# Kernel optimization log

Measured on AMD Instinct MI355X. Metric: run time of the kernel, lower is better.

## Reference

```python
import jax, jax.numpy as jnp
import numpy as np

N = 100000
E = 400000
NFEAT, NHID, NOUT, NHEAD = 128, 64, 128, 4
HIDDEN = NHID * NHEAD  # 256
SLOPE = 0.2


def gat_conv(x, src, dst, W, a_src, a_dst, b, concat):
    """PyG-style GATConv (eval mode, self-loops already appended to src/dst).
    x: [N, Fin]; W: [Fin, H*C]; a_src/a_dst: [H, C]; b: [H*C] or [C]."""
    H, C = a_src.shape
    h = (x @ W).reshape(N, H, C)                      # [N,H,C]
    al_s = (h * a_src).sum(-1)                        # [N,H] per-node src score
    al_d = (h * a_dst).sum(-1)                        # [N,H] per-node dst score
    e = jax.nn.leaky_relu(al_s[src] + al_d[dst], SLOPE)  # [Et,H]
    # segment softmax over incoming edges of each dst node
    m = jax.ops.segment_max(e, dst, num_segments=N)
    m = jnp.where(jnp.isfinite(m), m, 0.0)
    ex = jnp.exp(e - m[dst])
    denom = jax.ops.segment_sum(ex, dst, num_segments=N)
    alpha = ex / (denom[dst] + 1e-16)                 # [Et,H]
    msg = alpha[:, :, None] * h[src]                  # [Et,H,C]
    out = jax.ops.segment_sum(msg, dst, num_segments=N)  # [N,H,C]
    out = out.reshape(N, H * C) if concat else out.mean(axis=1)
    return out + b


def setup_inputs() -> dict:
    key = jax.random.key(0)
    ks = jax.random.split(key, 16)
    x = jax.random.normal(ks[0], (N, NFEAT), dtype=jnp.float32)
    edge_index = jax.random.randint(ks[1], (2, E), 0, N, dtype=jnp.int64)
    s = 0.1
    inp = {
        'x': x, 'edge_index': edge_index,
        # layer 0: nfeat -> nhid x nhead (concat)
        'W0': jax.random.normal(ks[2], (NFEAT, HIDDEN), jnp.float32) * s,
        'as0': jax.random.normal(ks[3], (NHEAD, NHID), jnp.float32) * s,
        'ad0': jax.random.normal(ks[4], (NHEAD, NHID), jnp.float32) * s,
        'b0': jnp.zeros((HIDDEN,), jnp.float32),
        # layer 1: hidden -> nhid x nhead (concat)
        'W1': jax.random.normal(ks[5], (HIDDEN, HIDDEN), jnp.float32) * s,
        'as1': jax.random.normal(ks[6], (NHEAD, NHID), jnp.float32) * s,
        'ad1': jax.random.normal(ks[7], (NHEAD, NHID), jnp.float32) * s,
        'b1': jnp.zeros((HIDDEN,), jnp.float32),
        # output layer: hidden -> nout, heads=1, concat=False
        'W2': jax.random.normal(ks[8], (HIDDEN, NOUT), jnp.float32) * s,
        'as2': jax.random.normal(ks[9], (1, NOUT), jnp.float32) * s,
        'ad2': jax.random.normal(ks[10], (1, NOUT), jnp.float32) * s,
        'b2': jnp.zeros((NOUT,), jnp.float32),
    }
    return inp


def reference(x, edge_index, W0, as0, ad0, b0, W1, as1, ad1, b1, W2, as2, ad2, b2):
    # PyG GATConv adds self-loops by default; edge set is shared across layers.
    loop = jnp.arange(N, dtype=edge_index.dtype)
    src = jnp.concatenate([edge_index[0], loop])
    dst = jnp.concatenate([edge_index[1], loop])
    # dropout inactive in eval mode
    h = jax.nn.elu(gat_conv(x, src, dst, W0, as0, ad0, b0, concat=True))
    h = jax.nn.elu(gat_conv(h, src, dst, W1, as1, ad1, b1, concat=True))
    out = gat_conv(h, src, dst, W2, as2, ad2, b2, concat=False)
    return out
```

## Files before the change

### kernel.cpp

```cpp
#include <hip/hip_runtime.h>
#include <cmath>

#define NN 100000
#define EE 400000
#define SLOPE 0.2f
#define MAXDEG 32

typedef __attribute__((ext_vector_type(8))) short short8;
typedef __attribute__((ext_vector_type(4))) float floatx4;

__device__ __forceinline__ float b2f(ushort u) {
    union { unsigned int i; float f; } v; v.i = ((unsigned int)u) << 16; return v.f;
}
__device__ __forceinline__ ushort f2b(float f) {
    union { float f; unsigned int i; } v; v.f = f;
    unsigned int r = v.i + 0x7FFFu + ((v.i >> 16) & 1u);
    return (ushort)(r >> 16);
}

__device__ __forceinline__ void gload16(const ushort* g, ushort* l) {
    __builtin_amdgcn_global_load_lds((const __attribute__((address_space(1))) void*)g,
                                     (__attribute__((address_space(3))) void*)l, 16, 0, 0);
}

__global__ __launch_bounds__(256) void prep(int* __restrict__ cnt,
                                            float* __restrict__ als2, float* __restrict__ ald2,
                                            const float* __restrict__ W0, const float* __restrict__ W1,
                                            const float* __restrict__ W2,
                                            ushort* __restrict__ Wt0, ushort* __restrict__ Wt1,
                                            ushort* __restrict__ Wt2) {
    int idx = blockIdx.x * 256 + threadIdx.x;
    if (idx < 25000) {
        ((int4*)cnt)[idx] = make_int4(0, 0, 0, 0);
    } else if (idx < 50000) {
        ((float4*)als2)[idx - 25000] = make_float4(0.f, 0.f, 0.f, 0.f);
    } else if (idx < 75000) {
        ((float4*)ald2)[idx - 50000] = make_float4(0.f, 0.f, 0.f, 0.f);
    } else {
        int j = idx - 75000;
        if (j < 32768) {
            int n = j >> 7, k = j & 127;
            Wt0[j] = f2b(W0[(size_t)k * 256 + n]);
        } else if (j < 98304) {
            int t = j - 32768;
            int n = t >> 8, k = t & 255;
            Wt1[t] = f2b(W1[(size_t)k * 256 + n]);
        } else if (j < 131072) {
            int t = j - 98304;
            int n = t >> 8, k = t & 255;
            Wt2[t] = f2b(W2[(size_t)k * 128 + n]);
        }
    }
}

__global__ __launch_bounds__(256) void bucket_scatter(const int* __restrict__ ei,
                                                      int* __restrict__ cnt,
                                                      int* __restrict__ bucket) {
    int e = blockIdx.x * 256 + threadIdx.x;
    if (e < EE) {
        int d = ei[EE + e];
        int p = atomicAdd(&cnt[d], 1);
        if (p < MAXDEG) bucket[(d << 5) + p] = ei[e];
    }
}

template <bool CVT>
__global__ __launch_bounds__(256) void gemm_bf16(const void* __restrict__ Avoid,
                                                 const ushort* __restrict__ Bt,
                                                 ushort* __restrict__ C,
                                                 int M, int K, int N, int paired,
                                                 const float* __restrict__ asf,
                                                 const float* __restrict__ adf,
                                                 float* __restrict__ als,
                                                 float* __restrict__ ald,
                                                 int H, int lgC) {
    __shared__ __attribute__((aligned(16))) ushort As[2 * 128 * 64];
    __shared__ __attribute__((aligned(16))) ushort Bs[2 * 128 * 64];
    int tid = threadIdx.x;
    int GMc = (M + 127) >> 7;
    int bmi, bni;
    if (paired) {
        int g = blockIdx.x >> 4, ii = blockIdx.x & 15;
        bmi = g * 8 + (ii & 7);
        bni = ii >> 3;
        if (bmi >= GMc) return;
    } else {
        bmi = blockIdx.x; bni = 0;
    }
    int bm = bmi * 128, bn = bni * 128;
    int wave = tid >> 6, lane = tid & 63;
    int wm = (wave >> 1) * 64, wn = (wave & 1) * 64;

    floatx4 acc[4][4];
#pragma unroll
    for (int i = 0; i < 4; i++)
#pragma unroll
        for (int j = 0; j < 4; j++) acc[i][j] = (floatx4)0.f;

    int rsub = lane >> 3;
    int klog8 = ((lane & 7) ^ rsub) * 8;
    ushort* ldsA = &As[wave * 512];
    ushort* ldsB = &Bs[wave * 512];
    const ushort* bS = Bt + (size_t)(bn + wave * 8 + rsub) * K + klog8;
    const ushort* aS = nullptr;
    if (!CVT) aS = (const ushort*)Avoid + (size_t)(bm + wave * 8 + rsub) * K + klog8;
    const float* Af = (const float*)Avoid;

    int frow = lane & 15;
    int q = lane >> 4;
    int f7 = frow & 7;

    int nt = K >> 6;
    int cur = 0;

    if constexpr (CVT) {
#pragma unroll
        for (int i = 0; i < 4; i++) {
            int arow = bm + wave * 8 + i * 32 + rsub;
            float4 f0 = make_float4(0.f, 0.f, 0.f, 0.f), f1 = f0;
            if (arow < M) {
                const float4* ap = (const float4*)(Af + (size_t)arow * K + klog8);
                f0 = ap[0]; f1 = ap[1];
            }
            uint4 pk;
            pk.x = (uint)f2b(f0.x) | ((uint)f2b(f0.y) << 16);
            pk.y = (uint)f2b(f0.z) | ((uint)f2b(f0.w) << 16);
            pk.z = (uint)f2b(f1.x) | ((uint)f2b(f1.y) << 16);
            pk.w = (uint)f2b(f1.z) | ((uint)f2b(f1.w) << 16);
            *(uint4*)&ldsA[i * 2048 + lane * 8] = pk;
            gload16(bS + (size_t)i * 32 * K, ldsB + i * 2048);
        }
    } else {
#pragma unroll
        for (int i = 0; i < 4; i++) {
            gload16(aS + (size_t)i * 32 * K, ldsA + i * 2048);
            gload16(bS + (size_t)i * 32 * K, ldsB + i * 2048);
        }
    }
    __syncthreads();

    for (int t = 0; t < nt; t++) {
        bool pre = (t + 1 < nt);
        int k0n = (t + 1) << 6;
        int nofs = (cur ^ 1) * 8192;

        float4 g0[4], g1[4];
        if constexpr (CVT) {
            if (pre) {
#pragma unroll
                for (int i = 0; i < 4; i++) {
                    int arow = bm + wave * 8 + i * 32 + rsub;
                    g0[i] = make_float4(0.f, 0.f, 0.f, 0.f); g1[i] = g0[i];
                    if (arow < M) {
                        const float4* ap = (const float4*)(Af + (size_t)arow * K + k0n + klog8);
                        g0[i] = ap[0]; g1[i] = ap[1];
                    }
                    gload16(bS + (size_t)i * 32 * K + k0n, ldsB + nofs + i * 2048);
                }
            }
        } else {
            if (pre) {
#pragma unroll
                for (int i = 0; i < 4; i++) {
                    gload16(aS + (size_t)i * 32 * K + k0n, ldsA + nofs + i * 2048);
                    gload16(bS + (size_t)i * 32 * K + k0n, ldsB + nofs + i * 2048);
                }
            }
        }

        {
            int bofs = cur * 8192;
#pragma unroll
            for (int kk = 0; kk < 2; kk++) {
                short8 afr[4], bfr[4];
                int phys = ((kk * 4 + q) ^ f7) * 8;
#pragma unroll
                for (int i = 0; i < 4; i++)
                    afr[i] = *(const short8*)&As[bofs + (wm + i * 16 + frow) * 64 + phys];
#pragma unroll
                for (int j = 0; j < 4; j++)
                    bfr[j] = *(const short8*)&Bs[bofs + (wn + j * 16 + frow) * 64 + phys];
#pragma unroll
                for (int i = 0; i < 4; i++)
#pragma unroll
                    for (int j = 0; j < 4; j++)
                        acc[i][j] = __builtin_amdgcn_mfma_f32_16x16x32_bf16(afr[i], bfr[j], acc[i][j], 0, 0, 0);
            }
        }

        if constexpr (CVT) {
            if (pre) {
#pragma unroll
                for (int i = 0; i < 4; i++) {
                    uint4 pk;
                    pk.x = (uint)f2b(g0[i].x) | ((uint)f2b(g0[i].y) << 16);
                    pk.y = (uint)f2b(g0[i].z) | ((uint)f2b(g0[i].w) << 16);
                    pk.z = (uint)f2b(g1[i].x) | ((uint)f2b(g1[i].y) << 16);
                    pk.w = (uint)f2b(g1[i].z) | ((uint)f2b(g1[i].w) << 16);
                    *(uint4*)&ldsA[nofs + i * 2048 + lane * 8] = pk;
                }
            }
        }

        __syncthreads();
        cur ^= 1;
    }

    int ccol = bn + wn + (lane & 15);
    int crow = bm + wm + (lane >> 4) * 4;
#pragma unroll
    for (int i = 0; i < 4; i++) {
#pragma unroll
        for (int reg = 0; reg < 4; reg++) {
            int row = crow + i * 16 + reg;
            if (row < M) {
#pragma unroll
                for (int j = 0; j < 4; j++)
                    C[(size_t)row * N + ccol + j * 16] = f2b(acc[i][j][reg]);
            }
        }
    }

    {
        int cb = bn + wn + (lane & 15);
        float asv[4], adv[4];
#pragma unroll
        for (int j = 0; j < 4; j++) {
            asv[j] = asf[cb + j * 16];
            adv[j] = adf[cb + j * 16];
        }
        int hidx = (bn + wn) >> lgC;
#pragma unroll
        for (int i = 0; i < 4; i++) {
#pragma unroll
            for (int reg = 0; reg < 4; reg++) {
                float ss = acc[i][0][reg] * asv[0] + acc[i][1][reg] * asv[1]
                         + acc[i][2][reg] * asv[2] + acc[i][3][reg] * asv[3];
                float dd = acc[i][0][reg] * adv[0] + acc[i][1][reg] * adv[1]
                         + acc[i][2][reg] * adv[2] + acc[i][3][reg] * adv[3];
#pragma unroll
                for (int off = 1; off < 16; off <<= 1) {
                    ss += __shfl_xor(ss, off, 64);
                    dd += __shfl_xor(dd, off, 64);
                }
                int row = crow + i * 16 + reg;
                if ((lane & 15) == 0 && row < M) {
                    if (lgC == 6) {
                        als[row * H + hidx] = ss;
                        ald[row * H + hidx] = dd;
                    } else {
                        atomicAdd(&als[row], ss);
                        atomicAdd(&ald[row], dd);
                    }
                }
            }
        }
    }
}

template <int H, int HC, bool ELU_ACT, bool OUT_BF16>
__global__ __launch_bounds__(256) void aggregate(const ushort* __restrict__ hlin,
                                                 const float* __restrict__ als,
                                                 const float* __restrict__ ald,
                                                 const int* __restrict__ cnt,
                                                 const int* __restrict__ bucket,
                                                 const float* __restrict__ bias,
                                                 void* __restrict__ outv) {
    constexpr int CP = HC / 64;
    constexpr int GS = 64 / H;
    int wv = threadIdx.x >> 6, lane = threadIdx.x & 63;
    int dst = blockIdx.x * 4 + wv;
    if (dst >= NN) return;
    int deg = min(cnt[dst], MAXDEG);
    int dtot = deg + 1;
    int rs = dst << 5;
    int eg = lane & (GS - 1);
    int head = lane / GS;
    float ad = ald[dst * H + head];

    float acc[CP];
#pragma unroll
    for (int j = 0; j < CP; j++) acc[j] = 0.f;

    uint laneoff = (uint)(lane * CP);

    if (dtot <= GS) {
        int src = 0;
        float s = -1e30f;
        if (eg < dtot) {
            src = (eg < deg) ? bucket[rs + eg] : dst;
            float sc = als[src * H + head] + ad;
            s = sc > 0.f ? sc : SLOPE * sc;
        }
        float m = s;
#pragma unroll
        for (int off = 1; off < GS; off <<= 1) m = fmaxf(m, __shfl_xor(m, off, 64));
        float e = (eg < dtot) ? __expf(s - m) : 0.f;
        float sum = e;
#pragma unroll
        for (int off = 1; off < GS; off <<= 1) sum += __shfl_xor(sum, off, 64);
        float w = e * (1.0f / (sum + 1e-16f));

        int hbase = head * GS;
        int d = 0;
        for (; d + 4 <= dtot; d += 4) {
            int s0 = __shfl(src, d, 64),     s1 = __shfl(src, d + 1, 64);
            int s2 = __shfl(src, d + 2, 64), s3 = __shfl(src, d + 3, 64);
            float w0 = __shfl(w, hbase + d, 64),     w1 = __shfl(w, hbase + d + 1, 64);
            float w2 = __shfl(w, hbase + d + 2, 64), w3 = __shfl(w, hbase + d + 3, 64);
            const uint* p0 = (const uint*)(hlin + (uint)s0 * HC + laneoff);
            const uint* p1 = (const uint*)(hlin + (uint)s1 * HC + laneoff);
            const uint* p2 = (const uint*)(hlin + (uint)s2 * HC + laneoff);
            const uint* p3 = (const uint*)(hlin + (uint)s3 * HC + laneoff);
            uint u0[CP / 2], u1[CP / 2], u2[CP / 2], u3[CP / 2];
#pragma unroll
            for (int qq = 0; qq < CP / 2; qq++) { u0[qq] = p0[qq]; u1[qq] = p1[qq]; u2[qq] = p2[qq]; u3[qq] = p3[qq]; }
#pragma unroll
            for (int qq = 0; qq < CP / 2; qq++) {
                acc[2*qq]   += w0 * b2f((ushort)(u0[qq] & 0xffff)) + w1 * b2f((ushort)(u1[qq] & 0xffff))
                             + w2 * b2f((ushort)(u2[qq] & 0xffff)) + w3 * b2f((ushort)(u3[qq] & 0xffff));
                acc[2*qq+1] += w0 * b2f((ushort)(u0[qq] >> 16)) + w1 * b2f((ushort)(u1[qq] >> 16))
                             + w2 * b2f((ushort)(u2[qq] >> 16)) + w3 * b2f((ushort)(u3[qq] >> 16));
            }
        }
        for (; d < dtot; d++) {
            int sd = __shfl(src, d, 64);
            float wd = __shfl(w, hbase + d, 64);
            const uint* p = (const uint*)(hlin + (uint)sd * HC + laneoff);
#pragma unroll
            for (int qq = 0; qq < CP / 2; qq++) {
                uint u = p[qq];
                acc[2*qq]   += wd * b2f((ushort)(u & 0xffff));
                acc[2*qq+1] += wd * b2f((ushort)(u >> 16));
            }
        }
    } else {
        float m = -1e30f;
        for (int e2 = eg; e2 < dtot; e2 += GS) {
            int s0 = (e2 < deg) ? bucket[rs + e2] : dst;
            float sc = als[s0 * H + head] + ad;
            sc = sc > 0.f ? sc : SLOPE * sc;
            m = fmaxf(m, sc);
        }
#pragma unroll
        for (int off = 1; off < GS; off <<= 1) m = fmaxf(m, __shfl_xor(m, off, 64));
        float sum = 0.f;
        for (int e2 = eg; e2 < dtot; e2 += GS) {
            int s0 = (e2 < deg) ? bucket[rs + e2] : dst;
            float sc = als[s0 * H + head] + ad;
            sc = sc > 0.f ? sc : SLOPE * sc;
            sum += __expf(sc - m);
        }
#pragma unroll
        for (int off = 1; off < GS; off <<= 1) sum += __shfl_xor(sum, off, 64);
        float inv = 1.0f / (sum + 1e-16f);
        for (int d = 0; d < dtot; d++) {
            int sd = (d < deg) ? bucket[rs + d] : dst;
            float sc = als[sd * H + head] + ad;
            sc = sc > 0.f ? sc : SLOPE * sc;
            float wd = __expf(sc - m) * inv;
            const uint* p = (const uint*)(hlin + (uint)sd * HC + laneoff);
#pragma unroll
            for (int qq = 0; qq < CP / 2; qq++) {
                uint u = p[qq];
                acc[2*qq]   += wd * b2f((ushort)(u & 0xffff));
                acc[2*qq+1] += wd * b2f((ushort)(u >> 16));
            }
        }
    }

#pragma unroll
    for (int j = 0; j < CP; j++) {
        float v = acc[j] + bias[lane * CP + j];
        if (ELU_ACT) v = v > 0.f ? v : (__expf(v) - 1.0f);
        acc[j] = v;
    }
    if (OUT_BF16) {
        ushort* outp = (ushort*)outv + (size_t)dst * HC + laneoff;
        uint pk[CP / 2];
#pragma unroll
        for (int qq = 0; qq < CP / 2; qq++)
            pk[qq] = (uint)f2b(acc[2*qq]) | ((uint)f2b(acc[2*qq+1]) << 16);
#pragma unroll
        for (int qq = 0; qq < CP / 2; qq++) ((uint*)outp)[qq] = pk[qq];
    } else {
        float* outp = (float*)outv + (size_t)dst * HC + laneoff;
#pragma unroll
        for (int j = 0; j < CP; j++) outp[j] = acc[j];
    }
}

extern "C" void kernel_launch(void* const* d_in, const int* in_sizes, int n_in,
                              void* d_out, int out_size, void* d_ws, size_t ws_size,
                              hipStream_t stream) {
    const float* x   = (const float*)d_in[0];
    const int*   ei  = (const int*)d_in[1];
    const float* W0  = (const float*)d_in[2];
    const float* as0 = (const float*)d_in[3];
    const float* ad0 = (const float*)d_in[4];
    const float* b0  = (const float*)d_in[5];
    const float* W1  = (const float*)d_in[6];
    const float* as1 = (const float*)d_in[7];
    const float* ad1 = (const float*)d_in[8];
    const float* b1  = (const float*)d_in[9];
    const float* W2  = (const float*)d_in[10];
    const float* as2 = (const float*)d_in[11];
    const float* ad2 = (const float*)d_in[12];
    const float* b2  = (const float*)d_in[13];
    float* out = (float*)d_out;

    char* ws = (char*)d_ws;
    size_t off = 0;
    auto alloc = [&](size_t bytes) {
        void* p = ws + off;
        off += (bytes + 255) & ~(size_t)255;
        return p;
    };
    ushort* h    = (ushort*)alloc((size_t)NN * 256 * 2);
    ushort* actB = (ushort*)alloc((size_t)(NN + 128) * 256 * 2);
    ushort* actC = (ushort*)alloc((size_t)(NN + 128) * 256 * 2);
    ushort* Wt0  = (ushort*)alloc((size_t)256 * 128 * 2);
    ushort* Wt1  = (ushort*)alloc((size_t)256 * 256 * 2);
    ushort* Wt2  = (ushort*)alloc((size_t)128 * 256 * 2);
    float* als   = (float*)alloc((size_t)NN * 4 * 4);
    float* ald   = (float*)alloc((size_t)NN * 4 * 4);
    float* als2  = (float*)alloc((size_t)NN * 4);
    float* ald2  = (float*)alloc((size_t)NN * 4);
    int* cnt     = (int*)alloc((size_t)NN * 4);
    int* bucket  = (int*)alloc((size_t)NN * MAXDEG * 4);

    prep<<<(75000 + 131072 + 255) / 256, 256, 0, stream>>>(cnt, als2, ald2, W0, W1, W2, Wt0, Wt1, Wt2);

    bucket_scatter<<<(EE + 255) / 256, 256, 0, stream>>>(ei, cnt, bucket);

    const int GMc = (NN + 127) / 128;
    const int GPAIR = 16 * ((GMc + 7) / 8);
    const int NB4 = (NN + 3) / 4;

    gemm_bf16<true><<<GPAIR, 256, 0, stream>>>(x, Wt0, h, NN, 128, 256, 1, as0, ad0, als, ald, 4, 6);
    aggregate<4, 256, true, true><<<NB4, 256, 0, stream>>>(h, als, ald, cnt, bucket, b0, actB);

    gemm_bf16<false><<<GPAIR, 256, 0, stream>>>(actB, Wt1, h, NN, 256, 256, 1, as1, ad1, als, ald, 4, 6);
    aggregate<4, 256, true, true><<<NB4, 256, 0, stream>>>(h, als, ald, cnt, bucket, b1, actC);

    gemm_bf16<false><<<GMc, 256, 0, stream>>>(actC, Wt2, h, NN, 256, 128, 0, as2, ad2, als2, ald2, 1, 7);
    aggregate<1, 128, false, false><<<NB4, 256, 0, stream>>>(h, als2, ald2, cnt, bucket, b2, out);
}
```

Measured before the change: 420.6 us.

## Make GEMMs persistent with the full weight tile resident in LDS

Replaces the per-tile GEMM with a persistent kernel. Each block loads its whole 128-column slice of the transposed weight matrix into LDS once, then grid-strides over M tiles, double-buffering only the activation tiles. Prefetch crosses tile boundaries, so the pipeline stays fed from one M tile to the next. This removes the repeated weight reloads from global memory and cuts the per-block launch and prologue overhead. In exchange it uses a large LDS footprint (up to 96 KB), which limits each CU to about one block, and it relies on a fixed grid size.

```diff
diff --git a/kernel.cpp b/kernel.cpp
--- a/kernel.cpp
+++ b/kernel.cpp
@@ -64,172 +64,171 @@
     }
 }
 
-template <bool CVT>
-__global__ __launch_bounds__(256) void gemm_bf16(const void* __restrict__ Avoid,
-                                                 const ushort* __restrict__ Bt,
-                                                 ushort* __restrict__ C,
-                                                 int M, int K, int N, int paired,
-                                                 const float* __restrict__ asf,
-                                                 const float* __restrict__ adf,
-                                                 float* __restrict__ als,
-                                                 float* __restrict__ ald,
-                                                 int H, int lgC) {
+template <bool CVT, int KT>
+__global__ __launch_bounds__(256) void gemm_nb(const void* __restrict__ Avoid,
+                                               const ushort* __restrict__ Bt,
+                                               ushort* __restrict__ C,
+                                               int M, int N, int nsplit,
+                                               const float* __restrict__ asf,
+                                               const float* __restrict__ adf,
+                                               float* __restrict__ als,
+                                               float* __restrict__ ald,
+                                               int H, int lgC) {
+    constexpr int SPR = KT / 8;
+    __shared__ __attribute__((aligned(16))) ushort Bs[128 * KT];
     __shared__ __attribute__((aligned(16))) ushort As[2 * 128 * 64];
-    __shared__ __attribute__((aligned(16))) ushort Bs[2 * 128 * 64];
     int tid = threadIdx.x;
-    int GMc = (M + 127) >> 7;
-    int bmi, bni;
-    if (paired) {
-        int g = blockIdx.x >> 4, ii = blockIdx.x & 15;
-        bmi = g * 8 + (ii & 7);
-        bni = ii >> 3;
-        if (bmi >= GMc) return;
-    } else {
-        bmi = blockIdx.x; bni = 0;
-    }
-    int bm = bmi * 128, bn = bni * 128;
     int wave = tid >> 6, lane = tid & 63;
-    int wm = (wave >> 1) * 64, wn = (wave & 1) * 64;
-
-    floatx4 acc[4][4];
-#pragma unroll
-    for (int i = 0; i < 4; i++)
-#pragma unroll
-        for (int j = 0; j < 4; j++) acc[i][j] = (floatx4)0.f;
+    int bid = blockIdx.x;
+    int bn, mslot, mstride;
+    if (nsplit) { bn = (bid >> 3) & 1; mslot = ((bid >> 4) << 3) + (bid & 7); mstride = gridDim.x >> 1; }
+    else        { bn = 0; mslot = bid; mstride = gridDim.x; }
+    int n0 = bn << 7;
+    int MT = (M + 127) >> 7;
 
     int rsub = lane >> 3;
     int klog8 = ((lane & 7) ^ rsub) * 8;
-    ushort* ldsA = &As[wave * 512];
-    ushort* ldsB = &Bs[wave * 512];
-    const ushort* bS = Bt + (size_t)(bn + wave * 8 + rsub) * K + klog8;
-    const ushort* aS = nullptr;
-    if (!CVT) aS = (const ushort*)Avoid + (size_t)(bm + wave * 8 + rsub) * K + klog8;
-    const float* Af = (const float*)Avoid;
-
     int frow = lane & 15;
     int q = lane >> 4;
     int f7 = frow & 7;
-
-    int nt = K >> 6;
-    int cur = 0;
-
-    if constexpr (CVT) {
-#pragma unroll
-        for (int i = 0; i < 4; i++) {
-            int arow = bm + wave * 8 + i * 32 + rsub;
-            float4 f0 = make_float4(0.f, 0.f, 0.f, 0.f), f1 = f0;
-            if (arow < M) {
-                const float4* ap = (const float4*)(Af + (size_t)arow * K + klog8);
-                f0 = ap[0]; f1 = ap[1];
-            }
-            uint4 pk;
-            pk.x = (uint)f2b(f0.x) | ((uint)f2b(f0.y) << 16);
-            pk.y = (uint)f2b(f0.z) | ((uint)f2b(f0.w) << 16);
-            pk.z = (uint)f2b(f1.x) | ((uint)f2b(f1.y) << 16);
-            pk.w = (uint)f2b(f1.z) | ((uint)f2b(f1.w) << 16);
-            *(uint4*)&ldsA[i * 2048 + lane * 8] = pk;
-            gload16(bS + (size_t)i * 32 * K, ldsB + i * 2048);
-        }
-    } else {
-#pragma unroll
-        for (int i = 0; i < 4; i++) {
-            gload16(aS + (size_t)i * 32 * K, ldsA + i * 2048);
-            gload16(bS + (size_t)i * 32 * K, ldsB + i * 2048);
+    int wm = (wave >> 1) * 64, wn = (wave & 1) * 64;
+
+    const float*  Af = (const float*)Avoid;
+    const ushort* Ab = (const ushort*)Avoid;
+
+    {
+        const ushort* Bt0 = Bt + (size_t)n0 * KT;
+#pragma unroll
+        for (int it = 0; it < SPR / 2; ++it) {
+            int sl = it * 256 + tid;
+            int br = sl / SPR;
+            int sc = sl & (SPR - 1);
+            int gc = sc ^ (br & 7);
+            gload16(Bt0 + (size_t)br * KT + gc * 8, &Bs[(it * 256 + wave * 64) * 8]);
+        }
+    }
+
+    floatx4 acc[4][4];
+#pragma unroll
+    for (int i = 0; i < 4; i++)
+#pragma unroll
+        for (int j = 0; j < 4; j++) acc[i][j] = (floatx4)0.f;
+
+    float asv[4], adv[4];
+#pragma unroll
+    for (int j = 0; j < 4; j++) {
+        asv[j] = asf[n0 + wn + (lane & 15) + j * 16];
+        adv[j] = adf[n0 + wn + (lane & 15) + j * 16];
+    }
+    int hidx = (n0 + wn) >> 6;
+
+    {
+        int bm = mslot << 7;
+        if constexpr (CVT) {
+#pragma unroll
+            for (int i = 0; i < 4; i++) {
+                int arow = bm + wave * 8 + i * 32 + rsub;
+                float4 f0 = make_float4(0.f, 0.f, 0.f, 0.f), f1 = f0;
+                if (arow < M) {
+                    const float4* ap = (const float4*)(Af + (size_t)arow * KT + klog8);
+                    f0 = ap[0]; f1 = ap[1];
+                }
+                uint4 pk;
+                pk.x = (uint)f2b(f0.x) | ((uint)f2b(f0.y) << 16);
+                pk.y = (uint)f2b(f0.z) | ((uint)f2b(f0.w) << 16);
+                pk.z = (uint)f2b(f1.x) | ((uint)f2b(f1.y) << 16);
+                pk.w = (uint)f2b(f1.z) | ((uint)f2b(f1.w) << 16);
+                *(uint4*)&As[wave * 512 + i * 2048 + lane * 8] = pk;
+            }
+        } else {
+#pragma unroll
+            for (int i = 0; i < 4; i++)
+                gload16(Ab + (size_t)(bm + wave * 8 + i * 32 + rsub) * KT + klog8,
+                        &As[wave * 512 + i * 2048]);
         }
     }
     __syncthreads();
 
-    for (int t = 0; t < nt; t++) {
-        bool pre = (t + 1 < nt);
-        int k0n = (t + 1) << 6;
-        int nofs = (cur ^ 1) * 8192;
-
-        float4 g0[4], g1[4];
-        if constexpr (CVT) {
+    int bufc = 0;
+    for (int t = mslot; t < MT; t += mstride) {
+        int bm = t << 7;
+#pragma unroll
+        for (int kc = 0; kc < KT / 64; ++kc) {
+            int nt_t = t, nt_kc = kc + 1;
+            if (nt_kc == KT / 64) { nt_t = t + mstride; nt_kc = 0; }
+            bool pre = (nt_t < MT);
+            int nb = bufc ^ 1;
+            float4 g0[4], g1[4];
+
             if (pre) {
-#pragma unroll
-                for (int i = 0; i < 4; i++) {
-                    int arow = bm + wave * 8 + i * 32 + rsub;
-                    g0[i] = make_float4(0.f, 0.f, 0.f, 0.f); g1[i] = g0[i];
-                    if (arow < M) {
-                        const float4* ap = (const float4*)(Af + (size_t)arow * K + k0n + klog8);
-                        g0[i] = ap[0]; g1[i] = ap[1];
+                int nbm = nt_t << 7;
+                if constexpr (CVT) {
+#pragma unroll
+                    for (int i = 0; i < 4; i++) {
+                        int arow = nbm + wave * 8 + i * 32 + rsub;
+                        g0[i] = make_float4(0.f, 0.f, 0.f, 0.f); g1[i] = g0[i];
+                        if (arow < M) {
+                            const float4* ap = (const float4*)(Af + (size_t)arow * KT + nt_kc * 64 + klog8);
+                            g0[i] = ap[0]; g1[i] = ap[1];
+                        }
                     }
-                    gload16(bS + (size_t)i * 32 * K + k0n, ldsB + nofs + i * 2048);
-                }
-            }
-        } else {
-            if (pre) {
-#pragma unroll
-                for (int i = 0; i < 4; i++) {
-                    gload16(aS + (size_t)i * 32 * K + k0n, ldsA + nofs + i * 2048);
-                    gload16(bS + (size_t)i * 32 * K + k0n, ldsB + nofs + i * 2048);
-                }
-            }
-        }
-
-        {
-            int bofs = cur * 8192;
+                } else {
+#pragma unroll
+                    for (int i = 0; i < 4; i++)
+                        gload16(Ab + (size_t)(nbm + wave * 8 + i * 32 + rsub) * KT + nt_kc * 64 + klog8,
+                                &As[nb * 8192 + wave * 512 + i * 2048]);
+                }
+            }
+
 #pragma unroll
             for (int kk = 0; kk < 2; kk++) {
                 short8 afr[4], bfr[4];
-                int phys = ((kk * 4 + q) ^ f7) * 8;
+                int ph = ((kk * 4 + q) ^ f7) * 8;
 #pragma unroll
                 for (int i = 0; i < 4; i++)
-                    afr[i] = *(const short8*)&As[bofs + (wm + i * 16 + frow) * 64 + phys];
+                    afr[i] = *(const short8*)&As[bufc * 8192 + (wm + i * 16 + frow) * 64 + ph];
 #pragma unroll
                 for (int j = 0; j < 4; j++)
-                    bfr[j] = *(const short8*)&Bs[bofs + (wn + j * 16 + frow) * 64 + phys];
+                    bfr[j] = *(const short8*)&Bs[(wn + j * 16 + frow) * KT + kc * 64 + ph];
 #pragma unroll
                 for (int i = 0; i < 4; i++)
 #pragma unroll
                     for (int j = 0; j < 4; j++)
                         acc[i][j] = __builtin_amdgcn_mfma_f32_16x16x32_bf16(afr[i], bfr[j], acc[i][j], 0, 0, 0);
             }
-        }
-
-        if constexpr (CVT) {
-            if (pre) {
-#pragma unroll
-                for (int i = 0; i < 4; i++) {
-                    uint4 pk;
-                    pk.x = (uint)f2b(g0[i].x) | ((uint)f2b(g0[i].y) << 16);
-                    pk.y = (uint)f2b(g0[i].z) | ((uint)f2b(g0[i].w) << 16);
-                    pk.z = (uint)f2b(g1[i].x) | ((uint)f2b(g1[i].y) << 16);
-                    pk.w = (uint)f2b(g1[i].z) | ((uint)f2b(g1[i].w) << 16);
-                    *(uint4*)&ldsA[nofs + i * 2048 + lane * 8] = pk;
-                }
-            }
-        }
-
-        __syncthreads();
-        cur ^= 1;
-    }
-
-    int ccol = bn + wn + (lane & 15);
-    int crow = bm + wm + (lane >> 4) * 4;
-#pragma unroll
-    for (int i = 0; i < 4; i++) {
-#pragma unroll
-        for (int reg = 0; reg < 4; reg++) {
-            int row = crow + i * 16 + reg;
-            if (row < M) {
-#pragma unroll
-                for (int j = 0; j < 4; j++)
-                    C[(size_t)row * N + ccol + j * 16] = f2b(acc[i][j][reg]);
-            }
-        }
-    }
-
-    {
-        int cb = bn + wn + (lane & 15);
-        float asv[4], adv[4];
-#pragma unroll
-        for (int j = 0; j < 4; j++) {
-            asv[j] = asf[cb + j * 16];
-            adv[j] = adf[cb + j * 16];
-        }
-        int hidx = (bn + wn) >> lgC;
+
+            if constexpr (CVT) {
+                if (pre) {
+#pragma unroll
+                    for (int i = 0; i < 4; i++) {
+                        uint4 pk;
+                        pk.x = (uint)f2b(g0[i].x) | ((uint)f2b(g0[i].y) << 16);
+                        pk.y = (uint)f2b(g0[i].z) | ((uint)f2b(g0[i].w) << 16);
+                        pk.z = (uint)f2b(g1[i].x) | ((uint)f2b(g1[i].y) << 16);
+                        pk.w = (uint)f2b(g1[i].z) | ((uint)f2b(g1[i].w) << 16);
+                        *(uint4*)&As[nb * 8192 + wave * 512 + i * 2048 + lane * 8] = pk;
+                    }
+                }
+            }
+
+            __syncthreads();
+            bufc ^= 1;
+        }
+
+        int ccol = n0 + wn + (lane & 15);
+        int crow = bm + wm + (lane >> 4) * 4;
+#pragma unroll
+        for (int i = 0; i < 4; i++) {
+#pragma unroll
+            for (int reg = 0; reg < 4; reg++) {
+                int row = crow + i * 16 + reg;
+                if (row < M) {
+#pragma unroll
+                    for (int j = 0; j < 4; j++)
+                        C[(size_t)row * N + ccol + j * 16] = f2b(acc[i][j][reg]);
+                }
+            }
+        }
 #pragma unroll
         for (int i = 0; i < 4; i++) {
 #pragma unroll
@@ -255,6 +254,10 @@
                 }
             }
         }
+#pragma unroll
+        for (int i = 0; i < 4; i++)
+#pragma unroll
+            for (int j = 0; j < 4; j++) acc[i][j] = (floatx4)0.f;
     }
 }
 
@@ -433,16 +436,14 @@
 
     bucket_scatter<<<(EE + 255) / 256, 256, 0, stream>>>(ei, cnt, bucket);
 
-    const int GMc = (NN + 127) / 128;
-    const int GPAIR = 16 * ((GMc + 7) / 8);
     const int NB4 = (NN + 3) / 4;
 
-    gemm_bf16<true><<<GPAIR, 256, 0, stream>>>(x, Wt0, h, NN, 128, 256, 1, as0, ad0, als, ald, 4, 6);
+    gemm_nb<true, 128><<<512, 256, 0, stream>>>(x, Wt0, h, NN, 256, 1, as0, ad0, als, ald, 4, 6);
     aggregate<4, 256, true, true><<<NB4, 256, 0, stream>>>(h, als, ald, cnt, bucket, b0, actB);
 
-    gemm_bf16<false><<<GPAIR, 256, 0, stream>>>(actB, Wt1, h, NN, 256, 256, 1, as1, ad1, als, ald, 4, 6);
+    gemm_nb<false, 256><<<256, 256, 0, stream>>>(actB, Wt1, h, NN, 256, 1, as1, ad1, als, ald, 4, 6);
     aggregate<4, 256, true, true><<<NB4, 256, 0, stream>>>(h, als, ald, cnt, bucket, b1, actC);
 
-    gemm_bf16<false><<<GMc, 256, 0, stream>>>(actC, Wt2, h, NN, 256, 128, 0, as2, ad2, als2, ald2, 1, 7);
+    gemm_nb<false, 256><<<256, 256, 0, stream>>>(actC, Wt2, h, NN, 128, 0, as2, ad2, als2, ald2, 1, 7);
     aggregate<1, 128, false, false><<<NB4, 256, 0, stream>>>(h, als2, ald2, cnt, bucket, b2, out);
 }
```

After: 429.1 us. 1.02x slower.
